# Optimization experiments

Measured on AMD Instinct MI355X. Metric: run time of the kernel, lower is better.

The kernel has to match this reference:

```python
import jax, jax.numpy as jnp
import numpy as np

N = 50000       # nodes
E = 1600000     # edges (avg degree 32)
D = 128         # in = hidden = out channels
H = 4           # attention heads


def setup_inputs() -> dict:
    key = jax.random.key(0)
    ks = jax.random.split(key, 9)
    s = 1.0 / np.sqrt(D)  # ~kaiming-scale linear weights
    return {
        "x": jax.random.normal(ks[0], (N, D), jnp.float32),
        "Wk": jax.random.normal(ks[1], (D, D), jnp.float32) * s,
        "bk": jnp.zeros((D,), jnp.float32),
        "Wq": jax.random.normal(ks[2], (D, D), jnp.float32) * s,
        "bq": jnp.zeros((D,), jnp.float32),
        "Wv": jax.random.normal(ks[3], (D, D), jnp.float32) * s,
        "bv": jnp.zeros((D,), jnp.float32),
        "src": jax.random.randint(ks[4], (E,), 0, N, dtype=jnp.int32),
        "dst": jax.random.randint(ks[5], (E,), 0, N, dtype=jnp.int32),
    }


def reference(x, Wk, bk, Wq, bq, Wv, bv, src, dst):
    n = x.shape[0]
    heads = H
    dk = Wk.shape[0] // heads
    dv = Wv.shape[0] // heads
    # Dense projections (near-roofline GEMMs)
    k = (x @ Wk.T + bk).reshape(n, heads, dk)
    q = (x @ Wq.T + bq).reshape(n, heads, dk)
    v = (x @ Wv.T + bv).reshape(n, heads, dv)
    # u_dot_v: per-edge per-head dot product (NO 1/sqrt(dk) scaling in source)
    scores = jnp.einsum('ehd,ehd->eh', k[src], q[dst])  # [E,H]
    # edge_softmax: softmax over incoming edges of each destination node
    m = jax.ops.segment_max(scores, dst, num_segments=n)        # [N,H]
    p = jnp.exp(scores - m[dst])                                 # [E,H]
    denom = jax.ops.segment_sum(p, dst, num_segments=n)         # [N,H]
    alpha = p / denom[dst]                                       # [E,H]
    # u_mul_e + sum: weighted scatter-aggregation of source values
    res = jax.ops.segment_sum(v[src] * alpha[:, :, None], dst, num_segments=n)  # [N,H,dv]
    # original: view(batch_size, -1, out_channels) with batch_size = N -> [N,1,out]
    return res.reshape(n, 1, heads * dv)
```

## Files before the change

### kernel.cpp

```cpp
#include <hip/hip_runtime.h>
#include <hip/hip_bf16.h>
#include <hip/hip_fp16.h>

#define NN 50000
#define NE 1600000
#define DD 128
#define HH 4
#define BSH2 5
#define NBKT2 1563
#define NBP2 2048
#define CAP 1408
#define PCHUNK 8192
#define NPB 196
#define GEMMB 782
#define MIDB (GEMMB + NPB)

typedef __attribute__((ext_vector_type(8))) short short8;
typedef __attribute__((ext_vector_type(4))) float floatx4;
typedef __attribute__((ext_vector_type(2))) _Float16 h2;

__device__ inline h2 as_h2(unsigned u) {
    union { unsigned u; h2 h; } c; c.u = u; return c.h;
}

__device__ inline float dot4(h2 a01, h2 a23, h2 b01, h2 b23) {
#if defined(__has_builtin) && __has_builtin(__builtin_amdgcn_fdot2)
    return __builtin_amdgcn_fdot2(a01, b01, __builtin_amdgcn_fdot2(a23, b23, 0.f, false), false);
#else
    return (float)a01.x * (float)b01.x + (float)a01.y * (float)b01.y +
           (float)a23.x * (float)b23.x + (float)a23.y * (float)b23.y;
#endif
}

__global__ __launch_bounds__(256) void prep_w(
    const float* __restrict__ Wk, const float* __restrict__ Wq, const float* __restrict__ Wv,
    unsigned short* __restrict__ hi, unsigned short* __restrict__ lo, int* __restrict__ bcur)
{
    int j = blockIdx.x * 256 + threadIdx.x;
    if (j < NBP2) bcur[j] = 0;
    if (j >= 3 * DD * DD) return;
    int which = j / (DD * DD);
    int off = j - which * (DD * DD);
    const float* W = (which == 0) ? Wk : (which == 1) ? Wq : Wv;
    float w = W[off];
    unsigned int b = __float_as_uint(w);
    unsigned short h = (unsigned short)(b >> 16);
    float hf = __uint_as_float((unsigned int)h << 16);
    float l = w - hf;
    hi[j] = h;
    lo[j] = (unsigned short)(__float_as_uint(l) >> 16);
}

__global__ __launch_bounds__(256) void mid(
    const float* __restrict__ x,
    const unsigned short* __restrict__ whi, const unsigned short* __restrict__ wlo,
    const float* __restrict__ bk, const float* __restrict__ bq, const float* __restrict__ bv,
    uint4* __restrict__ kvpack, __half* __restrict__ qh,
    const int* __restrict__ src, const int* __restrict__ dst,
    int* __restrict__ bcur, int* __restrict__ epack)
{
    __shared__ __align__(16) unsigned char smem[32768];

    if (blockIdx.x < GEMMB) {
        unsigned short (*stage)[4096] = (unsigned short (*)[4096])smem;
        int wave = threadIdx.x >> 6;
        int tile = blockIdx.x * 4 + wave;
        int n0 = tile * 16;
        if (n0 >= NN) return;
        int lane = threadIdx.x & 63;
        int m    = lane & 15;
        int quad = lane >> 4;

        const float* xrow = x + (size_t)(n0 + m) * DD + quad * 8;
        short8 ah[4], al[4];
#pragma unroll
        for (int ks = 0; ks < 4; ++ks) {
            const float* xr = xrow + ks * 32;
            float4 t0 = *(const float4*)xr;
            float4 t1 = *(const float4*)(xr + 4);
            float xv[8] = {t0.x, t0.y, t0.z, t0.w, t1.x, t1.y, t1.z, t1.w};
#pragma unroll
            for (int j = 0; j < 8; ++j) {
                unsigned int b = __float_as_uint(xv[j]);
                unsigned short h = (unsigned short)(b >> 16);
                float hf = __uint_as_float((unsigned int)h << 16);
                float l = xv[j] - hf;
                ah[ks][j] = (short)h;
                al[ks][j] = (short)(__float_as_uint(l) >> 16);
            }
        }

        floatx4 acc[3][8];
#pragma unroll
        for (int p = 0; p < 3; ++p)
#pragma unroll
            for (int ct = 0; ct < 8; ++ct)
                acc[p][ct] = (floatx4){0.f, 0.f, 0.f, 0.f};

#pragma unroll
        for (int ks = 0; ks < 4; ++ks) {
#pragma unroll
            for (int p = 0; p < 3; ++p) {
                size_t base = (size_t)p * DD * DD + (size_t)m * DD + ks * 32 + quad * 8;
#pragma unroll
                for (int ct = 0; ct < 8; ++ct) {
                    size_t o = base + (size_t)ct * 16 * DD;
                    short8 bh = *(const short8*)(whi + o);
                    short8 bl = *(const short8*)(wlo + o);
                    acc[p][ct] = __builtin_amdgcn_mfma_f32_16x16x32_bf16(ah[ks], bh, acc[p][ct], 0, 0, 0);
                    acc[p][ct] = __builtin_amdgcn_mfma_f32_16x16x32_bf16(ah[ks], bl, acc[p][ct], 0, 0, 0);
                    acc[p][ct] = __builtin_amdgcn_mfma_f32_16x16x32_bf16(al[ks], bh, acc[p][ct], 0, 0, 0);
                }
            }
        }

        int col = lane & 15;
        unsigned short* st = stage[wave];
        uint4* st4 = (uint4*)st;

#pragma unroll
        for (int ct = 0; ct < 8; ++ct) {
            int j = ct * 16 + col;
            int g = j >> 2, slot = j & 3;
            float biask = bk[j], biasv = bv[j];
#pragma unroll
            for (int r = 0; r < 4; ++r) {
                int row = quad * 4 + r;
                st[row * 256 + g * 8 + slot]     = __half_as_ushort(__float2half(acc[0][ct][r] + biask));
                st[row * 256 + g * 8 + 4 + slot] = __half_as_ushort(__float2half(acc[2][ct][r] + biasv));
            }
        }
#pragma unroll
        for (int t = 0; t < 8; ++t) {
            int flat = t * 64 + lane;
            kvpack[((size_t)n0 + (flat >> 5)) * 32 + (flat & 31)] = st4[flat];
        }

#pragma unroll
        for (int ct = 0; ct < 8; ++ct) {
            int j = ct * 16 + col;
            float biasq = bq[j];
#pragma unroll
            for (int r = 0; r < 4; ++r) {
                int row = quad * 4 + r;
                st[row * 128 + j] = __half_as_ushort(__float2half(acc[1][ct][r] + biasq));
            }
        }
#pragma unroll
        for (int t = 0; t < 4; ++t) {
            int flat = t * 64 + lane;
            ((uint4*)qh)[((size_t)n0 + (flat >> 4)) * 16 + (flat & 15)] = st4[flat];
        }
    } else {
        int* h  = (int*)smem;
        int* c2 = h + NBP2;
        int pb = blockIdx.x - GEMMB;
        int b0 = pb * PCHUNK;
        int n = min(PCHUNK, NE - b0);
        for (int i = threadIdx.x; i < NBP2; i += 256) h[i] = 0;
        __syncthreads();
        for (int i = threadIdx.x; i < n; i += 256)
            atomicAdd(&h[dst[b0 + i] >> BSH2], 1);
        __syncthreads();
        for (int i = threadIdx.x; i < NBP2; i += 256)
            c2[i] = h[i] ? i * CAP + atomicAdd(&bcur[i], h[i]) : 0;
        __syncthreads();
        for (int i = threadIdx.x; i < n; i += 256) {
            int d = dst[b0 + i];
            int s = src[b0 + i];
            int bkt = d >> BSH2;
            int pos = atomicAdd(&c2[bkt], 1);
            if (pos < (bkt + 1) * CAP)
                epack[pos] = ((d & 31) << 16) | s;
        }
    }
}

__global__ __launch_bounds__(256) void gat_bucket(
    const __half* __restrict__ qh, const uint4* __restrict__ kvpack,
    const int* __restrict__ epack, const int* __restrict__ bcur,
    float* __restrict__ out)
{
    __shared__ int hist[32];
    __shared__ int cur[32];
    __shared__ int begs[33];
    __shared__ unsigned short els[CAP];
    int b = blockIdx.x;
    int cnt = min(bcur[b], CAP);
    int base = b * CAP;
    int n0 = b << BSH2;
    int nnodes = min(32, NN - n0);
    int tid = threadIdx.x;

    if (tid < 32) hist[tid] = 0;
    __syncthreads();
    for (int e = tid; e < cnt; e += 256)
        atomicAdd(&hist[epack[base + e] >> 16], 1);
    __syncthreads();
    if (tid < 32) {
        int c = hist[tid], inc = c;
#pragma unroll
        for (int d = 1; d < 32; d <<= 1) {
            int t = __shfl_up(inc, d);
            if (tid >= d) inc += t;
        }
        int excl = inc - c;
        begs[tid] = excl;
        cur[tid]  = excl;
        if (tid == 31) begs[32] = excl + c;
    }
    __syncthreads();
    for (int e = tid; e < cnt; e += 256) {
        int p = epack[base + e];
        int pos = atomicAdd(&cur[p >> 16], 1);
        els[pos] = (unsigned short)(p & 0xFFFF);
    }
    __syncthreads();

    int il = tid & 31;
    int hw = tid >> 5;

    for (int nl = hw; nl < nnodes; nl += 8) {
        int node = n0 + nl;
        int beg = begs[nl], end = begs[nl + 1];

        uint2 qq = *(const uint2*)(qh + (size_t)node * 128 + il * 4);
        h2 qh01 = as_h2(qq.x), qh23 = as_h2(qq.y);

        float m = -INFINITY, ssum = 0.f;
        float o0 = 0.f, o1 = 0.f, o2 = 0.f, o3 = 0.f;

        for (int j = beg; j < end; j += 8) {
            int nh = min(8, end - j);
            uint4 kvv[8];
#pragma unroll
            for (int i = 0; i < 8; ++i) {
                int s = els[j + ((i < nh) ? i : 0)];
                kvv[i] = kvpack[(size_t)s * 32 + il];
            }
            float p[8];
#pragma unroll
            for (int i = 0; i < 8; ++i) {
                float t = dot4(as_h2(kvv[i].x), as_h2(kvv[i].y), qh01, qh23);
                t += __shfl_xor(t, 1);
                t += __shfl_xor(t, 2);
                t += __shfl_xor(t, 4);
                p[i] = (i < nh) ? t : -INFINITY;
            }
            float gm = fmaxf(fmaxf(fmaxf(p[0], p[1]), fmaxf(p[2], p[3])),
                             fmaxf(fmaxf(p[4], p[5]), fmaxf(p[6], p[7])));
            float nm = fmaxf(m, gm);
            float nmc = fmaxf(nm, -1e30f);
            float scale = __expf(m - nmc);
            ssum *= scale; o0 *= scale; o1 *= scale; o2 *= scale; o3 *= scale;
#pragma unroll
            for (int i = 0; i < 8; ++i) {
                float w = __expf(p[i] - nmc);
                ssum += w;
                o0 += w * (float)as_h2(kvv[i].z).x;
                o1 += w * (float)as_h2(kvv[i].z).y;
                o2 += w * (float)as_h2(kvv[i].w).x;
                o3 += w * (float)as_h2(kvv[i].w).y;
            }
            m = nm;
        }

        float invd = (ssum > 0.f) ? 1.f / ssum : 0.f;
        float4 r = {o0 * invd, o1 * invd, o2 * invd, o3 * invd};
        *(float4*)(out + (size_t)node * DD + il * 4) = r;
    }
}

extern "C" void kernel_launch(void* const* d_in, const int* in_sizes, int n_in,
                              void* d_out, int out_size, void* d_ws, size_t ws_size,
                              hipStream_t stream) {
    const float* x  = (const float*)d_in[0];
    const float* Wk = (const float*)d_in[1];
    const float* bk = (const float*)d_in[2];
    const float* Wq = (const float*)d_in[3];
    const float* bq = (const float*)d_in[4];
    const float* Wv = (const float*)d_in[5];
    const float* bv = (const float*)d_in[6];
    const int* src = (const int*)d_in[7];
    const int* dst = (const int*)d_in[8];

    uint4*  kvpack = (uint4*)d_ws;
    __half* qh     = (__half*)(kvpack + (size_t)NN * 32);
    unsigned short* whi = (unsigned short*)(qh + (size_t)NN * DD);
    unsigned short* wlo = whi + (size_t)3 * DD * DD;
    int* epack = (int*)(wlo + (size_t)3 * DD * DD);
    int* bcur  = epack + (size_t)NBKT2 * CAP;

    prep_w<<<(3 * DD * DD + 255) / 256, 256, 0, stream>>>(Wk, Wq, Wv, whi, wlo, bcur);
    mid<<<MIDB, 256, 0, stream>>>(x, whi, wlo, bk, bq, bv, kvpack, qh, src, dst, bcur, epack);
    gat_bucket<<<NBKT2, 256, 0, stream>>>(qh, kvpack, epack, bcur, (float*)d_out);
}
```

Measured before the change: 306.0 us.

## Restructure pipeline: precomputed histograms, persistent LDS-weight GEMM, ticketed prefetching GAT

Moves the per-chunk dst histogram into the prep kernel and writes it to global memory, so the partition blocks compute deterministic prefix offsets instead of using global atomics. The GEMM becomes persistent over 390 blocks. Each block stages one projection's hi weights in swizzled LDS and loops over tiles, and the K/V layout changes to separate k and v halves. The GAT kernel becomes persistent with an atomic ticket scheduler and software-prefetches the next 8 edges' K/V while computing the current batch. The serial prefix sum over up to 196 chunks per partition block and the lower GEMM parallelism may add latency.

```diff
diff --git a/kernel.cpp b/kernel.cpp
--- a/kernel.cpp
+++ b/kernel.cpp
@@ -12,8 +12,11 @@
 #define CAP 1408
 #define PCHUNK 8192
 #define NPB 196
-#define GEMMB 782
-#define MIDB (GEMMB + NPB)
+#define WPREPB 192
+#define PREPB (WPREPB + NPB)
+#define NGB 390
+#define MIDB (NGB + NPB)
+#define GATB 1024
 
 typedef __attribute__((ext_vector_type(8))) short short8;
 typedef __attribute__((ext_vector_type(4))) float floatx4;
@@ -32,140 +35,139 @@
 #endif
 }
 
-__global__ __launch_bounds__(256) void prep_w(
+__global__ __launch_bounds__(256) void prep(
     const float* __restrict__ Wk, const float* __restrict__ Wq, const float* __restrict__ Wv,
-    unsigned short* __restrict__ hi, unsigned short* __restrict__ lo, int* __restrict__ bcur)
+    unsigned short* __restrict__ hi, unsigned short* __restrict__ lo,
+    int* __restrict__ bcur, const int* __restrict__ dst, int* __restrict__ histg)
 {
-    int j = blockIdx.x * 256 + threadIdx.x;
-    if (j < NBP2) bcur[j] = 0;
-    if (j >= 3 * DD * DD) return;
-    int which = j / (DD * DD);
-    int off = j - which * (DD * DD);
-    const float* W = (which == 0) ? Wk : (which == 1) ? Wq : Wv;
-    float w = W[off];
-    unsigned int b = __float_as_uint(w);
-    unsigned short h = (unsigned short)(b >> 16);
-    float hf = __uint_as_float((unsigned int)h << 16);
-    float l = w - hf;
-    hi[j] = h;
-    lo[j] = (unsigned short)(__float_as_uint(l) >> 16);
+    __shared__ int h[NBP2];
+    if (blockIdx.x < WPREPB) {
+        int j = blockIdx.x * 256 + threadIdx.x;
+        if (j <= NBP2) bcur[j] = 0;
+        int which = j / (DD * DD);
+        int off = j - which * (DD * DD);
+        const float* W = (which == 0) ? Wk : (which == 1) ? Wq : Wv;
+        float w = W[off];
+        unsigned int b = __float_as_uint(w);
+        unsigned short hh = (unsigned short)(b >> 16);
+        float hf = __uint_as_float((unsigned int)hh << 16);
+        float l = w - hf;
+        hi[j] = hh;
+        lo[j] = (unsigned short)(__float_as_uint(l) >> 16);
+    } else {
+        int pb = blockIdx.x - WPREPB;
+        int b0 = pb * PCHUNK;
+        int n = min(PCHUNK, NE - b0);
+        for (int i = threadIdx.x; i < NBP2; i += 256) h[i] = 0;
+        __syncthreads();
+        for (int i = threadIdx.x; i < n; i += 256)
+            atomicAdd(&h[dst[b0 + i] >> BSH2], 1);
+        __syncthreads();
+        for (int i = threadIdx.x; i < NBP2; i += 256)
+            histg[(size_t)pb * NBP2 + i] = h[i];
+    }
 }
 
 __global__ __launch_bounds__(256) void mid(
     const float* __restrict__ x,
     const unsigned short* __restrict__ whi, const unsigned short* __restrict__ wlo,
     const float* __restrict__ bk, const float* __restrict__ bq, const float* __restrict__ bv,
-    uint4* __restrict__ kvpack, __half* __restrict__ qh,
+    uint4* __restrict__ kvpack, uint4* __restrict__ qh4,
     const int* __restrict__ src, const int* __restrict__ dst,
-    int* __restrict__ bcur, int* __restrict__ epack)
+    const int* __restrict__ histg, int* __restrict__ bcur, int* __restrict__ epack)
 {
-    __shared__ __align__(16) unsigned char smem[32768];
-
-    if (blockIdx.x < GEMMB) {
-        unsigned short (*stage)[4096] = (unsigned short (*)[4096])smem;
-        int wave = threadIdx.x >> 6;
-        int tile = blockIdx.x * 4 + wave;
-        int n0 = tile * 16;
-        if (n0 >= NN) return;
-        int lane = threadIdx.x & 63;
-        int m    = lane & 15;
-        int quad = lane >> 4;
-
-        const float* xrow = x + (size_t)(n0 + m) * DD + quad * 8;
-        short8 ah[4], al[4];
-#pragma unroll
-        for (int ks = 0; ks < 4; ++ks) {
-            const float* xr = xrow + ks * 32;
-            float4 t0 = *(const float4*)xr;
-            float4 t1 = *(const float4*)(xr + 4);
-            float xv[8] = {t0.x, t0.y, t0.z, t0.w, t1.x, t1.y, t1.z, t1.w};
-#pragma unroll
-            for (int j = 0; j < 8; ++j) {
-                unsigned int b = __float_as_uint(xv[j]);
-                unsigned short h = (unsigned short)(b >> 16);
-                float hf = __uint_as_float((unsigned int)h << 16);
-                float l = xv[j] - hf;
-                ah[ks][j] = (short)h;
-                al[ks][j] = (short)(__float_as_uint(l) >> 16);
-            }
-        }
-
-        floatx4 acc[3][8];
-#pragma unroll
-        for (int p = 0; p < 3; ++p)
-#pragma unroll
-            for (int ct = 0; ct < 8; ++ct)
-                acc[p][ct] = (floatx4){0.f, 0.f, 0.f, 0.f};
-
-#pragma unroll
-        for (int ks = 0; ks < 4; ++ks) {
-#pragma unroll
-            for (int p = 0; p < 3; ++p) {
-                size_t base = (size_t)p * DD * DD + (size_t)m * DD + ks * 32 + quad * 8;
+    __shared__ __align__(16) unsigned char smem[49152];
+
+    if (blockIdx.x < NGB) {
+        uint4* wl4 = (uint4*)smem;
+        int tid = threadIdx.x;
+        int wave = tid >> 6, lane = tid & 63;
+        int m = lane & 15, quad = lane >> 4;
+        unsigned short* st = (unsigned short*)(smem + 32768 + wave * 4096);
+        uint4* st4 = (uint4*)st;
+
+        for (int p = 0; p < 3; ++p) {
+            __syncthreads();
+            const uint4* gh = (const uint4*)whi + (size_t)p * 2048;
+            for (int g = tid; g < 2048; g += 256) {
+                int l = (g & ~15) | ((g ^ (g >> 4)) & 15);
+                wl4[l] = gh[g];
+            }
+            __syncthreads();
+            const float* bias = (p == 0) ? bk : (p == 1) ? bq : bv;
+            uint4* dbase = (p == 1) ? qh4 : kvpack;
+            int stride = (p == 1) ? 16 : 32;
+            int off    = (p == 2) ? 16 : 0;
+
+            for (int tile = blockIdx.x * 4 + wave; tile < 3125; tile += NGB * 4) {
+                int n0 = tile * 16;
+                const float* xrow = x + (size_t)(n0 + m) * DD + quad * 8;
+                short8 ah[4], al[4];
+#pragma unroll
+                for (int ks = 0; ks < 4; ++ks) {
+                    const float* xr = xrow + ks * 32;
+                    float4 t0 = *(const float4*)xr;
+                    float4 t1 = *(const float4*)(xr + 4);
+                    float xv[8] = {t0.x, t0.y, t0.z, t0.w, t1.x, t1.y, t1.z, t1.w};
+#pragma unroll
+                    for (int j = 0; j < 8; ++j) {
+                        unsigned int b = __float_as_uint(xv[j]);
+                        unsigned short h = (unsigned short)(b >> 16);
+                        float hf = __uint_as_float((unsigned int)h << 16);
+                        float l = xv[j] - hf;
+                        ah[ks][j] = (short)h;
+                        al[ks][j] = (short)(__float_as_uint(l) >> 16);
+                    }
+                }
+
+                floatx4 acc[8];
+#pragma unroll
+                for (int ct = 0; ct < 8; ++ct) acc[ct] = (floatx4){0.f, 0.f, 0.f, 0.f};
+
+#pragma unroll
+                for (int ks = 0; ks < 4; ++ks) {
+#pragma unroll
+                    for (int ct = 0; ct < 8; ++ct) {
+                        int r = ct * 16 + m;
+                        short8 bh = ((const short8*)wl4)[r * 16 + ((ks * 4 + quad) ^ m)];
+                        short8 bl = *(const short8*)(wlo + (size_t)p * 16384 +
+                                                     (size_t)r * 128 + ks * 32 + quad * 8);
+                        acc[ct] = __builtin_amdgcn_mfma_f32_16x16x32_bf16(ah[ks], bh, acc[ct], 0, 0, 0);
+                        acc[ct] = __builtin_amdgcn_mfma_f32_16x16x32_bf16(ah[ks], bl, acc[ct], 0, 0, 0);
+                        acc[ct] = __builtin_amdgcn_mfma_f32_16x16x32_bf16(al[ks], bh, acc[ct], 0, 0, 0);
+                    }
+                }
+
 #pragma unroll
                 for (int ct = 0; ct < 8; ++ct) {
-                    size_t o = base + (size_t)ct * 16 * DD;
-                    short8 bh = *(const short8*)(whi + o);
-                    short8 bl = *(const short8*)(wlo + o);
-                    acc[p][ct] = __builtin_amdgcn_mfma_f32_16x16x32_bf16(ah[ks], bh, acc[p][ct], 0, 0, 0);
-                    acc[p][ct] = __builtin_amdgcn_mfma_f32_16x16x32_bf16(ah[ks], bl, acc[p][ct], 0, 0, 0);
-                    acc[p][ct] = __builtin_amdgcn_mfma_f32_16x16x32_bf16(al[ks], bh, acc[p][ct], 0, 0, 0);
-                }
-            }
-        }
-
-        int col = lane & 15;
-        unsigned short* st = stage[wave];
-        uint4* st4 = (uint4*)st;
-
-#pragma unroll
-        for (int ct = 0; ct < 8; ++ct) {
-            int j = ct * 16 + col;
-            int g = j >> 2, slot = j & 3;
-            float biask = bk[j], biasv = bv[j];
-#pragma unroll
-            for (int r = 0; r < 4; ++r) {
-                int row = quad * 4 + r;
-                st[row * 256 + g * 8 + slot]     = __half_as_ushort(__float2half(acc[0][ct][r] + biask));
-                st[row * 256 + g * 8 + 4 + slot] = __half_as_ushort(__float2half(acc[2][ct][r] + biasv));
-            }
-        }
-#pragma unroll
-        for (int t = 0; t < 8; ++t) {
-            int flat = t * 64 + lane;
-            kvpack[((size_t)n0 + (flat >> 5)) * 32 + (flat & 31)] = st4[flat];
-        }
-
-#pragma unroll
-        for (int ct = 0; ct < 8; ++ct) {
-            int j = ct * 16 + col;
-            float biasq = bq[j];
-#pragma unroll
-            for (int r = 0; r < 4; ++r) {
-                int row = quad * 4 + r;
-                st[row * 128 + j] = __half_as_ushort(__float2half(acc[1][ct][r] + biasq));
-            }
-        }
-#pragma unroll
-        for (int t = 0; t < 4; ++t) {
-            int flat = t * 64 + lane;
-            ((uint4*)qh)[((size_t)n0 + (flat >> 4)) * 16 + (flat & 15)] = st4[flat];
+                    int j = ct * 16 + m;
+                    float bb = bias[j];
+#pragma unroll
+                    for (int r = 0; r < 4; ++r)
+                        st[(quad * 4 + r) * 128 + j] = __half_as_ushort(__float2half(acc[ct][r] + bb));
+                }
+#pragma unroll
+                for (int t = 0; t < 4; ++t) {
+                    int flat = t * 64 + lane;
+                    int row = flat >> 4, cc = flat & 15;
+                    dbase[(size_t)(n0 + row) * stride + off + cc] = st4[flat];
+                }
+            }
         }
     } else {
-        int* h  = (int*)smem;
-        int* c2 = h + NBP2;
-        int pb = blockIdx.x - GEMMB;
+        int* c2 = (int*)smem;
+        int pb = blockIdx.x - NGB;
+        int tid = threadIdx.x;
+        for (int i = tid; i < NBP2; i += 256) {
+            int s = 0;
+            for (int c = 0; c < pb; ++c) s += histg[(size_t)c * NBP2 + i];
+            if (pb == NPB - 1) bcur[i] = s + histg[(size_t)(NPB - 1) * NBP2 + i];
+            c2[i] = i * CAP + s;
+        }
+        __syncthreads();
         int b0 = pb * PCHUNK;
         int n = min(PCHUNK, NE - b0);
-        for (int i = threadIdx.x; i < NBP2; i += 256) h[i] = 0;
-        __syncthreads();
-        for (int i = threadIdx.x; i < n; i += 256)
-            atomicAdd(&h[dst[b0 + i] >> BSH2], 1);
-        __syncthreads();
-        for (int i = threadIdx.x; i < NBP2; i += 256)
-            c2[i] = h[i] ? i * CAP + atomicAdd(&bcur[i], h[i]) : 0;
-        __syncthreads();
-        for (int i = threadIdx.x; i < n; i += 256) {
+        for (int i = tid; i < n; i += 256) {
             int d = dst[b0 + i];
             int s = src[b0 + i];
             int bkt = d >> BSH2;
@@ -177,97 +179,126 @@
 }
 
 __global__ __launch_bounds__(256) void gat_bucket(
-    const __half* __restrict__ qh, const uint4* __restrict__ kvpack,
+    const __half* __restrict__ qh, const uint2* __restrict__ kv2,
     const int* __restrict__ epack, const int* __restrict__ bcur,
-    float* __restrict__ out)
+    int* __restrict__ ticket, float* __restrict__ out)
 {
     __shared__ int hist[32];
     __shared__ int cur[32];
     __shared__ int begs[33];
     __shared__ unsigned short els[CAP];
-    int b = blockIdx.x;
-    int cnt = min(bcur[b], CAP);
-    int base = b * CAP;
-    int n0 = b << BSH2;
-    int nnodes = min(32, NN - n0);
+    __shared__ int sb;
     int tid = threadIdx.x;
-
-    if (tid < 32) hist[tid] = 0;
-    __syncthreads();
-    for (int e = tid; e < cnt; e += 256)
-        atomicAdd(&hist[epack[base + e] >> 16], 1);
-    __syncthreads();
-    if (tid < 32) {
-        int c = hist[tid], inc = c;
-#pragma unroll
-        for (int d = 1; d < 32; d <<= 1) {
-            int t = __shfl_up(inc, d);
-            if (tid >= d) inc += t;
-        }
-        int excl = inc - c;
-        begs[tid] = excl;
-        cur[tid]  = excl;
-        if (tid == 31) begs[32] = excl + c;
-    }
-    __syncthreads();
-    for (int e = tid; e < cnt; e += 256) {
-        int p = epack[base + e];
-        int pos = atomicAdd(&cur[p >> 16], 1);
-        els[pos] = (unsigned short)(p & 0xFFFF);
-    }
-    __syncthreads();
-
     int il = tid & 31;
     int hw = tid >> 5;
 
-    for (int nl = hw; nl < nnodes; nl += 8) {
-        int node = n0 + nl;
-        int beg = begs[nl], end = begs[nl + 1];
-
-        uint2 qq = *(const uint2*)(qh + (size_t)node * 128 + il * 4);
-        h2 qh01 = as_h2(qq.x), qh23 = as_h2(qq.y);
-
-        float m = -INFINITY, ssum = 0.f;
-        float o0 = 0.f, o1 = 0.f, o2 = 0.f, o3 = 0.f;
-
-        for (int j = beg; j < end; j += 8) {
-            int nh = min(8, end - j);
-            uint4 kvv[8];
-#pragma unroll
-            for (int i = 0; i < 8; ++i) {
-                int s = els[j + ((i < nh) ? i : 0)];
-                kvv[i] = kvpack[(size_t)s * 32 + il];
-            }
-            float p[8];
-#pragma unroll
-            for (int i = 0; i < 8; ++i) {
-                float t = dot4(as_h2(kvv[i].x), as_h2(kvv[i].y), qh01, qh23);
-                t += __shfl_xor(t, 1);
-                t += __shfl_xor(t, 2);
-                t += __shfl_xor(t, 4);
-                p[i] = (i < nh) ? t : -INFINITY;
-            }
-            float gm = fmaxf(fmaxf(fmaxf(p[0], p[1]), fmaxf(p[2], p[3])),
-                             fmaxf(fmaxf(p[4], p[5]), fmaxf(p[6], p[7])));
-            float nm = fmaxf(m, gm);
-            float nmc = fmaxf(nm, -1e30f);
-            float scale = __expf(m - nmc);
-            ssum *= scale; o0 *= scale; o1 *= scale; o2 *= scale; o3 *= scale;
-#pragma unroll
-            for (int i = 0; i < 8; ++i) {
-                float w = __expf(p[i] - nmc);
-                ssum += w;
-                o0 += w * (float)as_h2(kvv[i].z).x;
-                o1 += w * (float)as_h2(kvv[i].z).y;
-                o2 += w * (float)as_h2(kvv[i].w).x;
-                o3 += w * (float)as_h2(kvv[i].w).y;
-            }
-            m = nm;
-        }
-
-        float invd = (ssum > 0.f) ? 1.f / ssum : 0.f;
-        float4 r = {o0 * invd, o1 * invd, o2 * invd, o3 * invd};
-        *(float4*)(out + (size_t)node * DD + il * 4) = r;
+    for (;;) {
+        __syncthreads();
+        if (tid == 0) sb = atomicAdd(ticket, 1);
+        __syncthreads();
+        int b = sb;
+        if (b >= NBKT2) return;
+
+        int cnt = min(bcur[b], CAP);
+        int base = b * CAP;
+        int n0 = b << BSH2;
+        int nnodes = min(32, NN - n0);
+
+        if (tid < 32) hist[tid] = 0;
+        __syncthreads();
+        for (int e = tid; e < cnt; e += 256)
+            atomicAdd(&hist[epack[base + e] >> 16], 1);
+        __syncthreads();
+        if (tid < 32) {
+            int c = hist[tid], inc = c;
+#pragma unroll
+            for (int d = 1; d < 32; d <<= 1) {
+                int t = __shfl_up(inc, d);
+                if (tid >= d) inc += t;
+            }
+            int excl = inc - c;
+            begs[tid] = excl;
+            cur[tid]  = excl;
+            if (tid == 31) begs[32] = excl + c;
+        }
+        __syncthreads();
+        for (int e = tid; e < cnt; e += 256) {
+            int p = epack[base + e];
+            int pos = atomicAdd(&cur[p >> 16], 1);
+            els[pos] = (unsigned short)(p & 0xFFFF);
+        }
+        __syncthreads();
+
+        for (int nl = hw; nl < nnodes; nl += 8) {
+            int node = n0 + nl;
+            int beg = begs[nl], end = begs[nl + 1];
+
+            uint2 qq = *(const uint2*)(qh + (size_t)node * 128 + il * 4);
+            h2 qh01 = as_h2(qq.x), qh23 = as_h2(qq.y);
+
+            float m = -INFINITY, ssum = 0.f;
+            float o0 = 0.f, o1 = 0.f, o2 = 0.f, o3 = 0.f;
+
+            uint2 kk[8], vv[8];
+            int nh = end - beg; if (nh > 8) nh = 8;
+            if (nh > 0) {
+#pragma unroll
+                for (int i = 0; i < 8; ++i) {
+                    int s = els[beg + ((i < nh) ? i : 0)];
+                    const uint2* pk = kv2 + (size_t)s * 64 + il;
+                    kk[i] = pk[0];
+                    vv[i] = pk[32];
+                }
+            }
+
+            for (int j = beg; j < end; j += 8) {
+                int jn = j + 8;
+                int rem = end - jn;
+                uint2 kn[8], vn[8];
+                if (rem > 0) {
+                    int nhc = (rem > 8) ? 8 : rem;
+#pragma unroll
+                    for (int i = 0; i < 8; ++i) {
+                        int s = els[jn + ((i < nhc) ? i : 0)];
+                        const uint2* pk = kv2 + (size_t)s * 64 + il;
+                        kn[i] = pk[0];
+                        vn[i] = pk[32];
+                    }
+                }
+                float p[8];
+#pragma unroll
+                for (int i = 0; i < 8; ++i) {
+                    float t = dot4(as_h2(kk[i].x), as_h2(kk[i].y), qh01, qh23);
+                    t += __shfl_xor(t, 1);
+                    t += __shfl_xor(t, 2);
+                    t += __shfl_xor(t, 4);
+                    p[i] = (i < nh) ? t : -INFINITY;
+                }
+                float gm = fmaxf(fmaxf(fmaxf(p[0], p[1]), fmaxf(p[2], p[3])),
+                                 fmaxf(fmaxf(p[4], p[5]), fmaxf(p[6], p[7])));
+                float nm = fmaxf(m, gm);
+                float nmc = fmaxf(nm, -1e30f);
+                float scale = __expf(m - nmc);
+                ssum *= scale; o0 *= scale; o1 *= scale; o2 *= scale; o3 *= scale;
+#pragma unroll
+                for (int i = 0; i < 8; ++i) {
+                    float w = __expf(p[i] - nmc);
+                    ssum += w;
+                    o0 += w * (float)as_h2(vv[i].x).x;
+                    o1 += w * (float)as_h2(vv[i].x).y;
+                    o2 += w * (float)as_h2(vv[i].y).x;
+                    o3 += w * (float)as_h2(vv[i].y).y;
+                }
+                m = nm;
+#pragma unroll
+                for (int i = 0; i < 8; ++i) { kk[i] = kn[i]; vv[i] = vn[i]; }
+                nh = (rem > 8) ? 8 : rem;
+            }
+
+            float invd = (ssum > 0.f) ? 1.f / ssum : 0.f;
+            float4 r = {o0 * invd, o1 * invd, o2 * invd, o3 * invd};
+            *(float4*)(out + (size_t)node * DD + il * 4) = r;
+        }
     }
 }
 
@@ -290,8 +321,11 @@
     unsigned short* wlo = whi + (size_t)3 * DD * DD;
     int* epack = (int*)(wlo + (size_t)3 * DD * DD);
     int* bcur  = epack + (size_t)NBKT2 * CAP;
-
-    prep_w<<<(3 * DD * DD + 255) / 256, 256, 0, stream>>>(Wk, Wq, Wv, whi, wlo, bcur);
-    mid<<<MIDB, 256, 0, stream>>>(x, whi, wlo, bk, bq, bv, kvpack, qh, src, dst, bcur, epack);
-    gat_bucket<<<NBKT2, 256, 0, stream>>>(qh, kvpack, epack, bcur, (float*)d_out);
-}
+    int* histg = bcur + (NBP2 + 1);
+
+    prep<<<PREPB, 256, 0, stream>>>(Wk, Wq, Wv, whi, wlo, bcur, dst, histg);
+    mid<<<MIDB, 256, 0, stream>>>(x, whi, wlo, bk, bq, bv, kvpack, (uint4*)qh,
+                                  src, dst, histg, bcur, epack);
+    gat_bucket<<<GATB, 256, 0, stream>>>(qh, (const uint2*)kvpack, epack, bcur,
+                                         bcur + NBP2, (float*)d_out);
+}
```

Result: slower. 441.0 us (+44.1%).
